# Performance work log

Measured on AMD Instinct MI355X. Metric: run time of the kernel, lower is better.

The kernel has to match this reference:

```python
import jax, jax.numpy as jnp
import numpy as np

K = 3  # sparsify_graph default k


def _lstm_dir(x, Wi, Wh, b, reverse):
    # x: [B, T, Hin]; Wi: [Hin, 4H]; Wh: [H, 4H]; b: [4H]
    B = x.shape[0]
    H = Wh.shape[0]
    xs = jnp.swapaxes(x, 0, 1)  # [T, B, Hin]
    if reverse:
        xs = xs[::-1]

    def step(carry, xt):
        h, c = carry
        g = xt @ Wi + h @ Wh + b
        i, f, gg, o = jnp.split(g, 4, axis=-1)  # torch gate order i,f,g,o
        c = jax.nn.sigmoid(f) * c + jax.nn.sigmoid(i) * jnp.tanh(gg)
        h = jax.nn.sigmoid(o) * jnp.tanh(c)
        return (h, c), h

    h0 = jnp.zeros((B, H), x.dtype)
    _, hs = jax.lax.scan(step, (h0, h0), xs)
    if reverse:
        hs = hs[::-1]
    return jnp.swapaxes(hs, 0, 1)  # [B, T, H]


def setup_inputs() -> dict:
    key = jax.random.key(0)
    ks = jax.random.split(key, 24)
    B, T, C, F = 16, 256, 64, 128
    GO, H = 32, 32  # gat_out, lstm hidden
    s = 0.1
    return {
        "x": jax.random.normal(ks[0], (B, T, C, F), jnp.float32),
        "spectral_w": jax.random.normal(ks[1], (C, F), jnp.float32),
        "gat_W": jax.random.normal(ks[2], (F, GO), jnp.float32) * s,
        "gat_a": jax.random.normal(ks[3], (2 * GO,), jnp.float32),
        "pool_w": jax.random.normal(ks[4], (GO, 1), jnp.float32) * s,
        "pool_b": jnp.zeros((1,), jnp.float32),
        "lstm_Wi_f": jax.random.normal(ks[5], (GO, 4 * H), jnp.float32) * s,
        "lstm_Wh_f": jax.random.normal(ks[6], (H, 4 * H), jnp.float32) * s,
        "lstm_b_f": jnp.zeros((4 * H,), jnp.float32),
        "lstm_Wi_r": jax.random.normal(ks[7], (GO, 4 * H), jnp.float32) * s,
        "lstm_Wh_r": jax.random.normal(ks[8], (H, 4 * H), jnp.float32) * s,
        "lstm_b_r": jnp.zeros((4 * H,), jnp.float32),
        "ta_W": jax.random.normal(ks[9], (2 * H, 2 * H), jnp.float32) * s,
        "ta_b": jnp.zeros((2 * H,), jnp.float32),
        "ta_v": jax.random.normal(ks[10], (2 * H,), jnp.float32) * s,
        "ln_g": jnp.ones((2 * H,), jnp.float32),
        "ln_b": jnp.zeros((2 * H,), jnp.float32),
        "fc1_w": jax.random.normal(ks[11], (2 * H, 32), jnp.float32) * s,
        "fc1_b": jnp.zeros((32,), jnp.float32),
        "fc2_w": jax.random.normal(ks[12], (32, 3), jnp.float32) * s,
        "fc2_b": jnp.zeros((3,), jnp.float32),
    }


def reference(x, spectral_w, gat_W, gat_a, pool_w, pool_b,
              lstm_Wi_f, lstm_Wh_f, lstm_b_f, lstm_Wi_r, lstm_Wh_r, lstm_b_r,
              ta_W, ta_b, ta_v, ln_g, ln_b, fc1_w, fc1_b, fc2_w, fc2_b):
    B, T, C, F = x.shape
    # SpectralWeighting: per-(channel,feature) softmaxed weights over feature dim
    x = x * jax.nn.softmax(spectral_w, axis=-1)  # [B,T,C,F]

    # compute_graph per sample: mean_t of cosine-similarity Gram over channels
    Hn = x / (jnp.linalg.norm(x, axis=-1, keepdims=True) + 1e-8)
    A = jnp.einsum('btcf,btdf->bcd', Hn, Hn) / T  # [B,C,C]

    # sparsify_graph: per-row top-(K+1), drop diagonal, symmetrize mask
    _, idx = jax.lax.top_k(A, K + 1)  # [B,C,K+1]
    topk_mask = jnp.sum(jax.nn.one_hot(idx, C, dtype=jnp.float32), axis=2) > 0  # [B,C,C]
    eye = jnp.eye(C, dtype=bool)
    topk_mask = topk_mask & ~eye
    topk_mask = topk_mask | jnp.swapaxes(topk_mask, 1, 2)
    A = jnp.where(topk_mask, A, 0.0)

    # GAT layer, vectorized over (B, T) with shared per-sample adjacency
    Wh = jnp.einsum('btcf,fo->btco', x, gat_W)  # [B,T,C,32]
    O = Wh.shape[-1]
    s1 = Wh @ gat_a[:O]  # [B,T,C]  a . Wh_i
    s2 = Wh @ gat_a[O:]  # [B,T,C]  a . Wh_j
    e = jax.nn.leaky_relu(s1[..., :, None] + s2[..., None, :], 0.2)  # [B,T,C,C]
    amask = (A > 0) | eye  # [B,C,C]
    e = jnp.where(amask[:, None], e, -1e9)
    alpha = jax.nn.softmax(e, axis=-1)  # dropout skipped (eval mode)
    gat = jax.nn.relu(jnp.einsum('btcd,btdo->btco', alpha, Wh))  # [B,T,C,32]

    # ChannelAttentionPooling: softmax over channel dim
    w = jax.nn.softmax(gat @ pool_w + pool_b, axis=2)  # [B,T,C,1]
    h = jnp.sum(gat * w, axis=2)  # [B,T,32]

    # BiLSTM
    hf = _lstm_dir(h, lstm_Wi_f, lstm_Wh_f, lstm_b_f, False)
    hr = _lstm_dir(h, lstm_Wi_r, lstm_Wh_r, lstm_b_r, True)
    h = jnp.concatenate([hf, hr], axis=-1)  # [B,T,64]

    # TemporalAttention (dropout skipped, eval mode)
    sc = (jnp.tanh(h @ ta_W + ta_b) @ ta_v) / 1.5  # [B,T]
    al = jax.nn.softmax(sc, axis=1)
    ctx = jnp.sum(h * al[..., None], axis=1)  # [B,64]

    # LayerNorm
    mu = jnp.mean(ctx, axis=-1, keepdims=True)
    var = jnp.var(ctx, axis=-1, keepdims=True)
    ctx = (ctx - mu) / jnp.sqrt(var + 1e-5) * ln_g + ln_b

    # Classifier head (dropout skipped, eval mode)
    return jax.nn.relu(ctx @ fc1_w + fc1_b) @ fc2_w + fc2_b  # [B,3]
```

## Files before the change

kernel.cpp:

```cpp
#include <hip/hip_runtime.h>
#include <hip/hip_bf16.h>

#define B_  16
#define T_  256
#define C_  64
#define F_  128
#define O_  32
#define H_  32
#define G4_ 128

typedef __attribute__((ext_vector_type(8))) short bfrag;
typedef __attribute__((ext_vector_type(4))) float f4acc;

__device__ __forceinline__ unsigned short f2bf(float v) {
    union { float f; unsigned u; } c; c.f = v;
    unsigned r = c.u + 0x7FFF + ((c.u >> 16) & 1);
    return (unsigned short)(r >> 16);
}
__device__ __forceinline__ float bf2f(unsigned short b) {
    union { float f; unsigned u; } c; c.u = ((unsigned)b) << 16; return c.f;
}
__device__ __forceinline__ float sigm_f(float x) {
    return __builtin_amdgcn_rcpf(1.f + __expf(-x));
}
__device__ __forceinline__ float tanh_f(float x) {
    float e = __expf(2.f * x);
    return 1.f - 2.f * __builtin_amdgcn_rcpf(e + 1.f);
}
__device__ __forceinline__ float readlane_f(float v, int l) {
    return __int_as_float(__builtin_amdgcn_readlane(__float_as_int(v), l));
}

__global__ __launch_bounds__(64) void k_sw(const float* __restrict__ w,
                                           float* __restrict__ sw) {
    int c = blockIdx.x, lane = threadIdx.x;
    const float* row = w + c * F_;
    float v0 = row[lane], v1 = row[lane + 64];
    float m = fmaxf(v0, v1);
#pragma unroll
    for (int s = 1; s < 64; s <<= 1) m = fmaxf(m, __shfl_xor(m, s));
    float e0 = __expf(v0 - m), e1 = __expf(v1 - m);
    float s = e0 + e1;
#pragma unroll
    for (int s_ = 1; s_ < 64; s_ <<= 1) s += __shfl_xor(s, s_);
    sw[c * F_ + lane] = e0 / s;
    sw[c * F_ + lane + 64] = e1 / s;
}

#define TCP 2
#define PSTR 136

#define MFMA16(a, b, c) __builtin_amdgcn_mfma_f32_16x16x32_bf16(a, b, c, 0, 0, 0)

__global__ __launch_bounds__(256) void k_phase1(
    const float* __restrict__ x, const float* __restrict__ sw,
    const float* __restrict__ gat_W, const float* __restrict__ gat_a,
    float* __restrict__ A, float* __restrict__ Wh,
    float* __restrict__ s1, float* __restrict__ s2) {
    const int b = blockIdx.x, tc = blockIdx.y, tid = threadIdx.x;
    const int wv = tid >> 6, lane = tid & 63;
    const int quad = lane >> 4, l16 = lane & 15;

    __shared__ unsigned short hhi[64 * PSTR];
    __shared__ unsigned short hlo[64 * PSTR];
    __shared__ float nrm[64];
    __shared__ float s1p[2][64], s2p[2][64];

    float4 swr[8];
    {
        const float4* sw4 = (const float4*)sw;
#pragma unroll
        for (int i = 0; i < 8; i++) swr[i] = sw4[tid + 256 * i];
    }

    const int rt0 = (wv >> 1) * 2;
    const int ct0 = (wv & 1) * 2;
    const int jW = wv & 1;

    bfrag wfh[4], wfl[4];
    {
        const int n = l16 + 16 * jW;
#pragma unroll
        for (int k = 0; k < 4; k++) {
            union { unsigned short u[8]; bfrag v; } Hu, Lu;
#pragma unroll
            for (int u = 0; u < 8; u++) {
                float v = gat_W[(32 * k + quad * 8 + u) * O_ + n];
                unsigned short hb = f2bf(v);
                Hu.u[u] = hb;
                Lu.u[u] = f2bf(v - bf2f(hb));
            }
            wfh[k] = Hu.v;
            wfl[k] = Lu.v;
        }
    }
    const float ga1 = gat_a[l16 + 16 * jW];
    const float ga2 = gat_a[O_ + l16 + 16 * jW];

    f4acc accA[2][2];
#pragma unroll
    for (int i = 0; i < 2; i++)
#pragma unroll
        for (int j = 0; j < 2; j++) accA[i][j] = (f4acc){0.f, 0.f, 0.f, 0.f};

    for (int tt = 0; tt < TCP; ++tt) {
        const int t = tc * TCP + tt;
        const float4* xg = (const float4*)(x + ((size_t)(b * T_ + t) << 13));
        float4 xr[8];
#pragma unroll
        for (int i = 0; i < 8; i++) xr[i] = xg[tid + 256 * i];

        float invn_[8];
#pragma unroll
        for (int i = 0; i < 8; i++) {
            float4 v = xr[i], s = swr[i];
            v.x *= s.x; v.y *= s.y; v.z *= s.z; v.w *= s.w;
            xr[i] = v;
            float ss = v.x * v.x + v.y * v.y + v.z * v.z + v.w * v.w;
#pragma unroll
            for (int d = 1; d < 32; d <<= 1) ss += __shfl_xor(ss, d);
            float nv = sqrtf(ss) + 1e-8f;
            invn_[i] = 1.0f / nv;
            if ((tid & 31) == 0) nrm[(tid >> 5) + 8 * i] = nv;
        }
#pragma unroll
        for (int i = 0; i < 8; i++) {
            int c = (tid >> 5) + 8 * i;
            float4 v = xr[i];
            float iv = invn_[i];
            float a0 = v.x * iv, a1 = v.y * iv, a2 = v.z * iv, a3 = v.w * iv;
            union { unsigned short u[4]; unsigned long long q; } Hq, Lq;
            unsigned short h0 = f2bf(a0), h1 = f2bf(a1), h2 = f2bf(a2), h3 = f2bf(a3);
            Hq.u[0] = h0; Hq.u[1] = h1; Hq.u[2] = h2; Hq.u[3] = h3;
            Lq.u[0] = f2bf(a0 - bf2f(h0));
            Lq.u[1] = f2bf(a1 - bf2f(h1));
            Lq.u[2] = f2bf(a2 - bf2f(h2));
            Lq.u[3] = f2bf(a3 - bf2f(h3));
            int off = c * PSTR + 4 * (tid & 31);
            *(unsigned long long*)&hhi[off] = Hq.q;
            *(unsigned long long*)&hlo[off] = Lq.q;
        }
        __syncthreads();

        f4acc accW0 = (f4acc){0.f, 0.f, 0.f, 0.f};
        f4acc accW1 = (f4acc){0.f, 0.f, 0.f, 0.f};
#pragma unroll
        for (int k = 0; k < 4; k++) {
            const int ko = 32 * k + 8 * quad;
            bfrag r0h = *(const bfrag*)&hhi[(rt0 * 16 + l16) * PSTR + ko];
            bfrag r0l = *(const bfrag*)&hlo[(rt0 * 16 + l16) * PSTR + ko];
            bfrag r1h = *(const bfrag*)&hhi[((rt0 + 1) * 16 + l16) * PSTR + ko];
            bfrag r1l = *(const bfrag*)&hlo[((rt0 + 1) * 16 + l16) * PSTR + ko];
            bfrag c0h = *(const bfrag*)&hhi[(ct0 * 16 + l16) * PSTR + ko];
            bfrag c0l = *(const bfrag*)&hlo[(ct0 * 16 + l16) * PSTR + ko];
            bfrag c1h = *(const bfrag*)&hhi[((ct0 + 1) * 16 + l16) * PSTR + ko];
            bfrag c1l = *(const bfrag*)&hlo[((ct0 + 1) * 16 + l16) * PSTR + ko];
            accA[0][0] = MFMA16(r0h, c0h, accA[0][0]);
            accA[0][0] = MFMA16(r0h, c0l, accA[0][0]);
            accA[0][0] = MFMA16(r0l, c0h, accA[0][0]);
            accA[0][1] = MFMA16(r0h, c1h, accA[0][1]);
            accA[0][1] = MFMA16(r0h, c1l, accA[0][1]);
            accA[0][1] = MFMA16(r0l, c1h, accA[0][1]);
            accA[1][0] = MFMA16(r1h, c0h, accA[1][0]);
            accA[1][0] = MFMA16(r1h, c0l, accA[1][0]);
            accA[1][0] = MFMA16(r1l, c0h, accA[1][0]);
            accA[1][1] = MFMA16(r1h, c1h, accA[1][1]);
            accA[1][1] = MFMA16(r1h, c1l, accA[1][1]);
            accA[1][1] = MFMA16(r1l, c1h, accA[1][1]);
            accW0 = MFMA16(r0h, wfh[k], accW0);
            accW0 = MFMA16(r0h, wfl[k], accW0);
            accW0 = MFMA16(r0l, wfh[k], accW0);
            accW1 = MFMA16(r1h, wfh[k], accW1);
            accW1 = MFMA16(r1h, wfl[k], accW1);
            accW1 = MFMA16(r1l, wfh[k], accW1);
        }
        float* whout = Wh + (size_t)(b * T_ + t) * (C_ * O_);
#pragma unroll
        for (int i2 = 0; i2 < 2; i2++) {
            f4acc aw = i2 ? accW1 : accW0;
#pragma unroll
            for (int r = 0; r < 4; r++) {
                int row = (rt0 + i2) * 16 + quad * 4 + r;
                float val = aw[r] * nrm[row];
                whout[row * O_ + l16 + 16 * jW] = val;
                float v1 = val * ga1, v2 = val * ga2;
#pragma unroll
                for (int d = 1; d < 16; d <<= 1) {
                    v1 += __shfl_xor(v1, d);
                    v2 += __shfl_xor(v2, d);
                }
                if (l16 == 0) { s1p[jW][row] = v1; s2p[jW][row] = v2; }
            }
        }
        __syncthreads();
        if (tid < 64) {
            s1[(b * T_ + t) * C_ + tid] = s1p[0][tid] + s1p[1][tid];
            s2[(b * T_ + t) * C_ + tid] = s2p[0][tid] + s2p[1][tid];
        }
    }
#pragma unroll
    for (int i2 = 0; i2 < 2; i2++)
#pragma unroll
        for (int j2 = 0; j2 < 2; j2++)
#pragma unroll
            for (int r = 0; r < 4; r++) {
                int row = (rt0 + i2) * 16 + quad * 4 + r;
                int col = (ct0 + j2) * 16 + l16;
                atomicAdd(&A[b * (C_ * C_) + row * C_ + col], accA[i2][j2][r]);
            }
}

__global__ __launch_bounds__(64) void k_topk(const float* __restrict__ A,
                                             unsigned long long* __restrict__ amask) {
    int b = blockIdx.x;
    int c = threadIdx.x;
    __shared__ unsigned long long tk[C_];
    const float* row = A + b * (C_ * C_) + c * C_;
    unsigned long long sel = 0ULL;
    for (int r = 0; r < 4; r++) {
        float best = -1e30f;
        int bi = 0;
        for (int d = 0; d < C_; d++) {
            if (sel & (1ULL << d)) continue;
            float v = row[d];
            if (v > best) { best = v; bi = d; }
        }
        sel |= (1ULL << bi);
    }
    unsigned long long t = sel & ~(1ULL << c);
    tk[c] = t;
    __syncthreads();
    unsigned long long sym = t;
    for (int d = 0; d < C_; d++)
        if ((tk[d] >> c) & 1ULL) sym |= (1ULL << d);
    unsigned long long m = (1ULL << c);
    unsigned long long s2 = sym;
    while (s2) {
        int d = __ffsll(s2) - 1;
        s2 &= s2 - 1;
        if (row[d] > 0.f) m |= (1ULL << d);
    }
    amask[b * C_ + c] = m;
}

__global__ __launch_bounds__(256) void k_gat(
    const float* __restrict__ Wh, const float* __restrict__ s1,
    const float* __restrict__ s2, const unsigned long long* __restrict__ amask,
    const float* __restrict__ pool_w, const float* __restrict__ pool_b,
    float* __restrict__ hout) {
    int tg = blockIdx.x;
    int wv = threadIdx.x >> 6, c = threadIdx.x & 63;
    int bt = tg * 4 + wv;
    int b = bt >> 8;
    __shared__ float buf[4][C_][33];
    __shared__ float s2s[4][C_];

    s2s[wv][c] = s2[bt * C_ + c];
    float s1c = s1[bt * C_ + c];
    unsigned long long m = amask[b * C_ + c];
    __syncthreads();

    float mx = -1e30f;
    unsigned long long mm = m;
    while (mm) {
        int d = __ffsll(mm) - 1; mm &= mm - 1;
        float v = s1c + s2s[wv][d];
        v = v > 0.f ? v : 0.2f * v;
        mx = fmaxf(mx, v);
    }
    float ssum = 0.f;
    mm = m;
    while (mm) {
        int d = __ffsll(mm) - 1; mm &= mm - 1;
        float v = s1c + s2s[wv][d];
        v = v > 0.f ? v : 0.2f * v;
        ssum += __expf(v - mx);
    }
    float inv = 1.0f / ssum;
    float g[O_];
#pragma unroll
    for (int i = 0; i < O_; i++) g[i] = 0.f;
    mm = m;
    while (mm) {
        int d = __ffsll(mm) - 1; mm &= mm - 1;
        float v = s1c + s2s[wv][d];
        v = v > 0.f ? v : 0.2f * v;
        float a = __expf(v - mx);
        const float4* wr = (const float4*)(Wh + (size_t)bt * (C_ * O_) + d * O_);
#pragma unroll
        for (int q = 0; q < 8; q++) {
            float4 w4 = wr[q];
            g[4 * q + 0] += a * w4.x;
            g[4 * q + 1] += a * w4.y;
            g[4 * q + 2] += a * w4.z;
            g[4 * q + 3] += a * w4.w;
        }
    }
    float lg = pool_b[0];
#pragma unroll
    for (int i = 0; i < O_; i++) {
        g[i] = fmaxf(g[i] * inv, 0.f);
        lg += g[i] * pool_w[i];
    }
    float wmx = lg;
#pragma unroll
    for (int s = 1; s < 64; s <<= 1) wmx = fmaxf(wmx, __shfl_xor(wmx, s));
    float we = __expf(lg - wmx);
    float wsum = we;
#pragma unroll
    for (int s = 1; s < 64; s <<= 1) wsum += __shfl_xor(wsum, s);
    float wcf = we / wsum;
#pragma unroll
    for (int i = 0; i < O_; i++) buf[wv][c][i] = g[i] * wcf;
    __syncthreads();
    {
        int wt = threadIdx.x >> 6, o = threadIdx.x & 31, hf = (threadIdx.x >> 5) & 1;
        float sacc = 0.f;
#pragma unroll 8
        for (int d = hf * 32; d < hf * 32 + 32; d++) sacc += buf[wt][d][o];
        sacc += __shfl_xor(sacc, 32);
        if (hf == 0) hout[(tg * 4 + wt) * O_ + o] = sacc;
    }
}

__global__ __launch_bounds__(128) void k_lstm_pre(
    const float* __restrict__ hin,
    const float* __restrict__ Wi_f, const float* __restrict__ b_f,
    const float* __restrict__ Wi_r, const float* __restrict__ b_r,
    float* __restrict__ gx) {
    int id = blockIdx.x;
    int dir = id >> 12;
    int bt = id & 4095;
    const float* Wi = dir ? Wi_r : Wi_f;
    const float* bb = dir ? b_r : b_f;
    int g = threadIdx.x;
    __shared__ float hs[H_];
    if (g < H_) hs[g] = hin[bt * O_ + g];
    __syncthreads();
    float acc = bb[g];
#pragma unroll
    for (int k = 0; k < H_; k++) acc += hs[k] * Wi[k * G4_ + g];
    gx[((size_t)dir * 4096 + bt) * G4_ + g] = acc;
}

#define WW(k) float2 ww##k = make_float2(Wd[(k) * G4_ + lane], Wd[(k) * G4_ + lane + 64]);
#define KST(k, Aq) { float hk = readlane_f(h, k); \
    Aq.x = fmaf(hk, ww##k.x, Aq.x); Aq.y = fmaf(hk, ww##k.y, Aq.y); }

__global__ void __attribute__((amdgpu_flat_work_group_size(64, 64)))
__attribute__((amdgpu_waves_per_eu(1, 1))) k_lstm_seq(
    const float* __restrict__ gx,
    const float* __restrict__ Whf, const float* __restrict__ Whr,
    float* __restrict__ hcat) {
    int dir = blockIdx.x & 1, b = blockIdx.x >> 1;
    int lane = threadIdx.x;
    const float* Wd = dir ? Whr : Whf;
    WW(0) WW(1) WW(2) WW(3) WW(4) WW(5) WW(6) WW(7)
    WW(8) WW(9) WW(10) WW(11) WW(12) WW(13) WW(14) WW(15)
    WW(16) WW(17) WW(18) WW(19) WW(20) WW(21) WW(22) WW(23)
    WW(24) WW(25) WW(26) WW(27) WW(28) WW(29) WW(30) WW(31)

    const float* gxb = gx + ((size_t)dir * 4096 + b * T_) * G4_;
    float h = 0.f, cst = 0.f;
    const int dt = dir ? -1 : 1;
    int t = dir ? (T_ - 1) : 0;
    float g0n = gxb[t * G4_ + lane], g1n = gxb[t * G4_ + lane + 64];
    const float half_sel = (lane < 32) ? 2.f : 1.f;
    for (int s = 0; s < T_; s++) {
        int tn = t + dt;
        float2 A0 = make_float2(g0n, g1n);
        float2 A1 = make_float2(0.f, 0.f);
        float2 A2 = make_float2(0.f, 0.f);
        float2 A3 = make_float2(0.f, 0.f);
        if (s < T_ - 1) {
            g0n = gxb[tn * G4_ + lane];
            g1n = gxb[tn * G4_ + lane + 64];
        }
        KST(0, A0)  KST(1, A1)  KST(2, A2)  KST(3, A3)
        KST(4, A0)  KST(5, A1)  KST(6, A2)  KST(7, A3)
        KST(8, A0)  KST(9, A1)  KST(10, A2) KST(11, A3)
        KST(12, A0) KST(13, A1) KST(14, A2) KST(15, A3)
        KST(16, A0) KST(17, A1) KST(18, A2) KST(19, A3)
        KST(20, A0) KST(21, A1) KST(22, A2) KST(23, A3)
        KST(24, A0) KST(25, A1) KST(26, A2) KST(27, A3)
        KST(28, A0) KST(29, A1) KST(30, A2) KST(31, A3)
        float g0 = (A0.x + A1.x) + (A2.x + A3.x);
        float g1 = (A0.y + A1.y) + (A2.y + A3.y);
        float sA = sigm_f(g0);
        float u = sigm_f(half_sel * g1);
        float sB = (lane < 32) ? fmaf(2.f, u, -1.f) : u;
        float sf = __shfl(sA, (lane & 31) + 32);
        float so = __shfl(sB, (lane & 31) + 32);
        cst = fmaf(sf, cst, sA * sB);
        float hn = so * tanh_f(cst);
        h = hn;
        if (lane < H_) hcat[((size_t)(b * T_) + t) * (2 * H_) + dir * H_ + lane] = hn;
        t = tn;
    }
}

__global__ __launch_bounds__(256) void k_final(
    const float* __restrict__ hcat,
    const float* __restrict__ taW, const float* __restrict__ tab,
    const float* __restrict__ tav,
    const float* __restrict__ lng, const float* __restrict__ lnb,
    const float* __restrict__ w1, const float* __restrict__ b1,
    const float* __restrict__ w2, const float* __restrict__ b2,
    float* __restrict__ out) {
    int b = blockIdx.x;
    int t = threadIdx.x;
    __shared__ float Wl[64 * 64];
    __shared__ float al[T_];
    __shared__ float wred[4];
    __shared__ float ctxp[4][64];
    __shared__ float ctx[64];
    __shared__ float a1[32];
    for (int i = t; i < 4096; i += 256) Wl[i] = taW[i];
    float4 hr[16];
    const float4* hb = (const float4*)(hcat + ((size_t)b * T_ + t) * 64);
#pragma unroll
    for (int i = 0; i < 16; i++) hr[i] = hb[i];
    __syncthreads();
    float sc = 0.f;
    for (int j = 0; j < 64; j++) {
        float s = tab[j];
#pragma unroll
        for (int k4 = 0; k4 < 16; k4++) {
            float4 h4 = hr[k4];
            const float* wcol = &Wl[(4 * k4) * 64 + j];
            s += h4.x * wcol[0] + h4.y * wcol[64] + h4.z * wcol[128] + h4.w * wcol[192];
        }
        sc += tanhf(s) * tav[j];
    }
    sc *= (1.0f / 1.5f);
    int wave = t >> 6, lane = t & 63;
    float m = sc;
#pragma unroll
    for (int s_ = 1; s_ < 64; s_ <<= 1) m = fmaxf(m, __shfl_xor(m, s_));
    if (lane == 0) wred[wave] = m;
    __syncthreads();
    m = fmaxf(fmaxf(wred[0], wred[1]), fmaxf(wred[2], wred[3]));
    float e = __expf(sc - m);
    float ssum = e;
#pragma unroll
    for (int s_ = 1; s_ < 64; s_ <<= 1) ssum += __shfl_xor(ssum, s_);
    __syncthreads();
    if (lane == 0) wred[wave] = ssum;
    __syncthreads();
    float S = wred[0] + wred[1] + wred[2] + wred[3];
    al[t] = e / S;
    __syncthreads();
    {
        int o = t & 63, part = t >> 6;
        float cacc = 0.f;
        for (int tt = part * 64; tt < part * 64 + 64; tt++)
            cacc += al[tt] * hcat[((size_t)b * T_ + tt) * 64 + o];
        ctxp[part][o] = cacc;
    }
    __syncthreads();
    if (t < 64) {
        float ctxo = ctxp[0][t] + ctxp[1][t] + ctxp[2][t] + ctxp[3][t];
        float sv = ctxo, sq = ctxo * ctxo;
#pragma unroll
        for (int s_ = 1; s_ < 64; s_ <<= 1) {
            sv += __shfl_xor(sv, s_);
            sq += __shfl_xor(sq, s_);
        }
        float mu = sv * (1.f / 64.f);
        float var = sq * (1.f / 64.f) - mu * mu;
        ctx[t] = (ctxo - mu) / sqrtf(var + 1e-5f) * lng[t] + lnb[t];
    }
    __syncthreads();
    if (t < 32) {
        float s = b1[t];
        for (int k = 0; k < 64; k++) s += ctx[k] * w1[k * 32 + t];
        a1[t] = fmaxf(s, 0.f);
    }
    __syncthreads();
    if (t < 3) {
        float s = b2[t];
        for (int k = 0; k < 32; k++) s += a1[k] * w2[k * 3 + t];
        out[b * 3 + t] = s;
    }
}

extern "C" void kernel_launch(void* const* d_in, const int* in_sizes, int n_in,
                              void* d_out, int out_size, void* d_ws, size_t ws_size,
                              hipStream_t stream) {
    const float* x          = (const float*)d_in[0];
    const float* spectral_w = (const float*)d_in[1];
    const float* gat_W      = (const float*)d_in[2];
    const float* gat_a      = (const float*)d_in[3];
    const float* pool_w     = (const float*)d_in[4];
    const float* pool_b     = (const float*)d_in[5];
    const float* lstm_Wi_f  = (const float*)d_in[6];
    const float* lstm_Wh_f  = (const float*)d_in[7];
    const float* lstm_b_f   = (const float*)d_in[8];
    const float* lstm_Wi_r  = (const float*)d_in[9];
    const float* lstm_Wh_r  = (const float*)d_in[10];
    const float* lstm_b_r   = (const float*)d_in[11];
    const float* ta_W       = (const float*)d_in[12];
    const float* ta_b       = (const float*)d_in[13];
    const float* ta_v       = (const float*)d_in[14];
    const float* ln_g       = (const float*)d_in[15];
    const float* ln_b       = (const float*)d_in[16];
    const float* fc1_w      = (const float*)d_in[17];
    const float* fc1_b      = (const float*)d_in[18];
    const float* fc2_w      = (const float*)d_in[19];
    const float* fc2_b      = (const float*)d_in[20];
    float* out = (float*)d_out;

    float* ws = (float*)d_ws;
    float* sw    = ws + 0;
    float* A     = ws + 8192;
    unsigned long long* amask = (unsigned long long*)(ws + 73728);
    float* Wh    = ws + 75776;
    float* s1    = ws + 8464384;
    float* s2    = ws + 8726528;
    float* hpool = ws + 8988672;
    float* gx    = ws + 9119744;
    float* hcat  = ws + 10168320;

    hipMemsetAsync(A, 0, (size_t)C_ * C_ * B_ * sizeof(float), stream);
    k_sw<<<C_, 64, 0, stream>>>(spectral_w, sw);
    k_phase1<<<dim3(B_, T_ / TCP), 256, 0, stream>>>(x, sw, gat_W, gat_a, A, Wh, s1, s2);
    k_topk<<<B_, 64, 0, stream>>>(A, amask);
    k_gat<<<B_ * T_ / 4, 256, 0, stream>>>(Wh, s1, s2, amask, pool_w, pool_b, hpool);
    k_lstm_pre<<<2 * B_ * T_, 128, 0, stream>>>(hpool, lstm_Wi_f, lstm_b_f,
                                                lstm_Wi_r, lstm_b_r, gx);
    k_lstm_seq<<<2 * B_, 64, 0, stream>>>(gx, lstm_Wh_f, lstm_Wh_r, hcat);
    k_final<<<B_, 256, 0, stream>>>(hcat, ta_W, ta_b, ta_v, ln_g, ln_b,
                                    fc1_w, fc1_b, fc2_w, fc2_b, out);
}
```

Measured before the change: 448.9 us.

## Fuse LSTM input projection into GAT kernel and pack LSTM recurrence FMAs

The LSTM input projection (hpool @ Wi + b for both directions) is folded into the tail of the GAT pooling kernel. Pooled features stay in shared memory and each thread computes four timesteps per weight load, which removes one kernel launch and the hpool round trip through global memory. The sequential LSTM loop now uses 2-wide float vectors with elementwise fma so the compiler can emit packed FMA instructions on the latency-bound recurrence. The cost is extra work and an added barrier in the GAT kernel.

```diff
diff --git a/kernel.cpp b/kernel.cpp
--- a/kernel.cpp
+++ b/kernel.cpp
@@ -11,6 +11,7 @@
 
 typedef __attribute__((ext_vector_type(8))) short bfrag;
 typedef __attribute__((ext_vector_type(4))) float f4acc;
+typedef __attribute__((ext_vector_type(2))) float f2v;
 
 __device__ __forceinline__ unsigned short f2bf(float v) {
     union { float f; unsigned u; } c; c.f = v;
@@ -247,13 +248,16 @@
     const float* __restrict__ Wh, const float* __restrict__ s1,
     const float* __restrict__ s2, const unsigned long long* __restrict__ amask,
     const float* __restrict__ pool_w, const float* __restrict__ pool_b,
-    float* __restrict__ hout) {
+    const float* __restrict__ Wi_f, const float* __restrict__ b_f,
+    const float* __restrict__ Wi_r, const float* __restrict__ b_r,
+    float* __restrict__ gx) {
     int tg = blockIdx.x;
     int wv = threadIdx.x >> 6, c = threadIdx.x & 63;
     int bt = tg * 4 + wv;
     int b = bt >> 8;
     __shared__ float buf[4][C_][33];
     __shared__ float s2s[4][C_];
+    __shared__ float hp[4][H_];
 
     s2s[wv][c] = s2[bt * C_ + c];
     float s1c = s1[bt * C_ + c];
@@ -319,33 +323,35 @@
 #pragma unroll 8
         for (int d = hf * 32; d < hf * 32 + 32; d++) sacc += buf[wt][d][o];
         sacc += __shfl_xor(sacc, 32);
-        if (hf == 0) hout[(tg * 4 + wt) * O_ + o] = sacc;
-    }
-}
-
-__global__ __launch_bounds__(128) void k_lstm_pre(
-    const float* __restrict__ hin,
-    const float* __restrict__ Wi_f, const float* __restrict__ b_f,
-    const float* __restrict__ Wi_r, const float* __restrict__ b_r,
-    float* __restrict__ gx) {
-    int id = blockIdx.x;
-    int dir = id >> 12;
-    int bt = id & 4095;
-    const float* Wi = dir ? Wi_r : Wi_f;
-    const float* bb = dir ? b_r : b_f;
-    int g = threadIdx.x;
-    __shared__ float hs[H_];
-    if (g < H_) hs[g] = hin[bt * O_ + g];
-    __syncthreads();
-    float acc = bb[g];
-#pragma unroll
-    for (int k = 0; k < H_; k++) acc += hs[k] * Wi[k * G4_ + g];
-    gx[((size_t)dir * 4096 + bt) * G4_ + g] = acc;
-}
-
-#define WW(k) float2 ww##k = make_float2(Wd[(k) * G4_ + lane], Wd[(k) * G4_ + lane + 64]);
+        if (hf == 0) hp[wt][o] = sacc;
+    }
+    __syncthreads();
+    {
+        int dir = threadIdx.x >> 7, col = threadIdx.x & 127;
+        const float* Wi = dir ? Wi_r : Wi_f;
+        const float* bb = dir ? b_r : b_f;
+        float bv = bb[col];
+        float a0 = bv, a1 = bv, a2 = bv, a3 = bv;
+#pragma unroll
+        for (int k = 0; k < H_; k++) {
+            float wvv = Wi[k * G4_ + col];
+            a0 = fmaf(hp[0][k], wvv, a0);
+            a1 = fmaf(hp[1][k], wvv, a1);
+            a2 = fmaf(hp[2][k], wvv, a2);
+            a3 = fmaf(hp[3][k], wvv, a3);
+        }
+        size_t base = (size_t)dir * 4096 + (size_t)tg * 4;
+        gx[(base + 0) * G4_ + col] = a0;
+        gx[(base + 1) * G4_ + col] = a1;
+        gx[(base + 2) * G4_ + col] = a2;
+        gx[(base + 3) * G4_ + col] = a3;
+    }
+}
+
+#define WW(k) f2v ww##k = (f2v){Wd[(k) * G4_ + lane], Wd[(k) * G4_ + lane + 64]};
 #define KST(k, Aq) { float hk = readlane_f(h, k); \
-    Aq.x = fmaf(hk, ww##k.x, Aq.x); Aq.y = fmaf(hk, ww##k.y, Aq.y); }
+    f2v hkv = (f2v){hk, hk}; \
+    Aq = __builtin_elementwise_fma(hkv, ww##k, Aq); }
 
 __global__ void __attribute__((amdgpu_flat_work_group_size(64, 64)))
 __attribute__((amdgpu_waves_per_eu(1, 1))) k_lstm_seq(
@@ -368,10 +374,10 @@
     const float half_sel = (lane < 32) ? 2.f : 1.f;
     for (int s = 0; s < T_; s++) {
         int tn = t + dt;
-        float2 A0 = make_float2(g0n, g1n);
-        float2 A1 = make_float2(0.f, 0.f);
-        float2 A2 = make_float2(0.f, 0.f);
-        float2 A3 = make_float2(0.f, 0.f);
+        f2v A0 = (f2v){g0n, g1n};
+        f2v A1 = (f2v){0.f, 0.f};
+        f2v A2 = (f2v){0.f, 0.f};
+        f2v A3 = (f2v){0.f, 0.f};
         if (s < T_ - 1) {
             g0n = gxb[tn * G4_ + lane];
             g1n = gxb[tn * G4_ + lane + 64];
@@ -384,8 +390,11 @@
         KST(20, A0) KST(21, A1) KST(22, A2) KST(23, A3)
         KST(24, A0) KST(25, A1) KST(26, A2) KST(27, A3)
         KST(28, A0) KST(29, A1) KST(30, A2) KST(31, A3)
-        float g0 = (A0.x + A1.x) + (A2.x + A3.x);
-        float g1 = (A0.y + A1.y) + (A2.y + A3.y);
+        f2v S01 = A0 + A1;
+        f2v S23 = A2 + A3;
+        f2v S = S01 + S23;
+        float g0 = S.x;
+        float g1 = S.y;
         float sA = sigm_f(g0);
         float u = sigm_f(half_sel * g1);
         float sB = (lane < 32) ? fmaf(2.f, u, -1.f) : u;
@@ -517,7 +526,6 @@
     float* Wh    = ws + 75776;
     float* s1    = ws + 8464384;
     float* s2    = ws + 8726528;
-    float* hpool = ws + 8988672;
     float* gx    = ws + 9119744;
     float* hcat  = ws + 10168320;
 
@@ -525,9 +533,8 @@
     k_sw<<<C_, 64, 0, stream>>>(spectral_w, sw);
     k_phase1<<<dim3(B_, T_ / TCP), 256, 0, stream>>>(x, sw, gat_W, gat_a, A, Wh, s1, s2);
     k_topk<<<B_, 64, 0, stream>>>(A, amask);
-    k_gat<<<B_ * T_ / 4, 256, 0, stream>>>(Wh, s1, s2, amask, pool_w, pool_b, hpool);
-    k_lstm_pre<<<2 * B_ * T_, 128, 0, stream>>>(hpool, lstm_Wi_f, lstm_b_f,
-                                                lstm_Wi_r, lstm_b_r, gx);
+    k_gat<<<B_ * T_ / 4, 256, 0, stream>>>(Wh, s1, s2, amask, pool_w, pool_b,
+                                           lstm_Wi_f, lstm_b_f, lstm_Wi_r, lstm_b_r, gx);
     k_lstm_seq<<<2 * B_, 64, 0, stream>>>(gx, lstm_Wh_f, lstm_Wh_r, hcat);
     k_final<<<B_, 256, 0, stream>>>(hcat, ta_W, ta_b, ta_v, ln_g, ln_b,
                                     fc1_w, fc1_b, fc2_w, fc2_b, out);
```

After: 463.2 us. 3.2% more time.
